# Kernel tuning notes

Measured on AMD Instinct MI355X. Metric: run time of the kernel, lower is better.

The kernel has to match this reference:

```python
import jax, jax.numpy as jnp
import numpy as np

WEIGHT = 1.0
TEMPERATURE = 1.0
POWER = 2.0
NEG_FILL = -1e9
EPS = 1e-8


def _cos_sim_matrix(x):
    # row-normalize then GEMM: equivalent to pairwise F.cosine_similarity
    norms = jnp.linalg.norm(x, axis=-1, keepdims=True)
    xn = x / jnp.maximum(norms, EPS)
    return xn @ xn.T  # [N, N]


def setup_inputs() -> dict:
    key = jax.random.key(0)
    k1, k2 = jax.random.split(key)
    model_output = jax.random.normal(k1, (8192, 512), dtype=jnp.float32)
    targets = jax.random.normal(k2, (8192, 768), dtype=jnp.float32)
    return {"model_output": model_output, "targets": targets}


def reference(model_output, targets):
    N = model_output.shape[0]
    eye = jnp.eye(N, dtype=bool)

    sim_o = jnp.where(eye, NEG_FILL, _cos_sim_matrix(model_output))
    sim_t = jnp.where(eye, NEG_FILL, _cos_sim_matrix(targets))

    student_log_probs = jax.nn.log_softmax(sim_o / TEMPERATURE, axis=-1)
    teacher_probs = jax.nn.softmax(sim_t / TEMPERATURE, axis=-1)

    weights = jax.lax.stop_gradient(teacher_probs ** POWER)

    # torch F.kl_div(input=log_p_student, target=p_teacher, reduction='none')
    # = where(target > 0, target * (log(target) - input), 0)
    tp_safe = jnp.where(teacher_probs > 0, teacher_probs, 1.0)
    kl = jnp.where(teacher_probs > 0,
                   teacher_probs * (jnp.log(tp_safe) - student_log_probs),
                   0.0)

    loss = jnp.mean(weights * kl)
    return WEIGHT * loss
```

## Files before the change

### kernel.cpp

```cpp
#include <hip/hip_runtime.h>

#define N    8192
#define DT   768
#define DO   512
#define BM   128
#define BN   128
#define TI   (N / BM)
#define TJ   (N / BN)
#define NTILE (TI * (TI + 1) / 2)
#define NSLOT (2 * TJ)
#define PL    ((size_t)NSLOT * N)
#define NKT   (DT / 32)
#define NKO   (DO / 32)

typedef __attribute__((ext_vector_type(8))) short   short8;
typedef __attribute__((ext_vector_type(4))) float   floatx4;

struct alignas(8) us4 { unsigned short x[4]; };

__device__ inline unsigned short f2bf(float x) {
    union { float f; unsigned int u; } v; v.f = x;
    unsigned int r = v.u + 0x7fffu + ((v.u >> 16) & 1u);
    return (unsigned short)(r >> 16);
}
__device__ inline float bf2f(unsigned short u) {
    union { unsigned int u; float f; } v; v.u = ((unsigned int)u) << 16;
    return v.f;
}

__device__ inline void gl2lds16(const unsigned short* g, unsigned short* l) {
    __builtin_amdgcn_global_load_lds(
        (const __attribute__((address_space(1))) unsigned int*)(const void*)g,
        (__attribute__((address_space(3))) unsigned int*)(void*)l,
        16, 0, 0);
}

template <int NKC>
__device__ inline void stage_packed(const unsigned short* __restrict__ P,
                                    unsigned short* sA, unsigned short* sB,
                                    int pi, int pj, int s, int t) {
    const unsigned short* bi = P + ((size_t)(pi * NKC + s) << 12);
    const unsigned short* bj = P + ((size_t)(pj * NKC + s) << 12);
    #pragma unroll
    for (int h = 0; h < 2; ++h) {
        const int idx = t + h * 256;
        gl2lds16(bi + idx * 8, &sA[idx * 8]);
        gl2lds16(bj + idx * 8, &sB[idx * 8]);
    }
}

__device__ inline void tile_coords(int bid, int& ti, int& tj) {
    int swb = (bid & 7) * (NTILE / 8) + (bid >> 3);
    int sti = 0, stj = 0;
    for (;;) {
        const int sz = (sti == stj) ? 36 : 64;
        if (swb < sz) break;
        swb -= sz;
        if (++stj == 8) { ++sti; stj = sti; }
    }
    int i, j;
    if (sti == stj) {
        i = 0;
        while (swb >= 8 - i) { swb -= 8 - i; ++i; }
        j = i + swb;
    } else {
        i = swb >> 3;
        j = swb & 7;
    }
    ti = sti * 8 + i;
    tj = stj * 8 + j;
}

__global__ void norm_kernel(const float* __restrict__ Tg,
                            const float* __restrict__ Mo,
                            unsigned short* __restrict__ Pt,
                            unsigned short* __restrict__ Po,
                            float* __restrict__ zero_me) {
    if (blockIdx.x == 0 && threadIdx.x == 0) zero_me[0] = 0.0f;
    int bid = blockIdx.x;
    const float* X; unsigned short* Pk; int D, NKC;
    if (bid < N / 4) { X = Tg; Pk = Pt; D = DT; NKC = NKT; }
    else             { bid -= N / 4; X = Mo; Pk = Po; D = DO; NKC = NKO; }
    const int row  = bid * 4 + (threadIdx.x >> 6);
    const int lane = threadIdx.x & 63;
    const int nch  = D >> 8;
    const int r    = row & 127;
    const int p    = row >> 7;
    const int key  = (r >> 1) & 3;
    const float* xr = X + (size_t)row * D;
    floatx4 vc[3];
    float ss = 0.0f;
    #pragma unroll
    for (int h = 0; h < 3; ++h) {
        if (h < nch) {
            vc[h] = *(const floatx4*)(xr + lane * 4 + h * 256);
            ss += vc[h][0] * vc[h][0] + vc[h][1] * vc[h][1]
                + vc[h][2] * vc[h][2] + vc[h][3] * vc[h][3];
        }
    }
    #pragma unroll
    for (int m = 32; m >= 1; m >>= 1) ss += __shfl_xor(ss, m);
    const float scale = 1.0f / fmaxf(sqrtf(ss), 1e-8f);
    #pragma unroll
    for (int h = 0; h < 3; ++h) {
        if (h < nch) {
            us4 o;
            #pragma unroll
            for (int j = 0; j < 4; ++j) o.x[j] = f2bf(vc[h][j] * scale);
            const int k0  = lane * 4 + h * 256;
            const int kc  = k0 >> 5;
            const int ch  = (k0 >> 3) & 3;
            const int cs  = ch ^ key;
            const int pos = (k0 >> 2) & 1;
            const size_t a = ((size_t)(p * NKC + kc) << 12)
                           + (size_t)(r * 4 + cs) * 8 + pos * 4;
            *(us4*)(Pk + a) = o;
        }
    }
}

__launch_bounds__(256, 3)
__global__ void fused_kernel(const unsigned short* __restrict__ Pt,
                             const unsigned short* __restrict__ Po,
                             float* __restrict__ partials) {
    __shared__ unsigned short sA[BM * 32];
    __shared__ unsigned short sB[BN * 32];
    __shared__ unsigned short sW[64 * 256];

    const int t    = threadIdx.x;
    const int lane = t & 63;
    const int w    = t >> 6;
    const int wm   = w >> 1, wn = w & 1;
    const int lr   = lane & 15, lg = lane >> 4;
    const int lgx  = lg ^ ((lr >> 1) & 3);

    int ti, tj; tile_coords(blockIdx.x, ti, tj);
    const bool offdiag = (ti != tj);
    const int i0 = ti * BM, j0 = tj * BN;

    floatx4 acc[4][4];
    #pragma unroll
    for (int a = 0; a < 4; ++a)
        #pragma unroll
        for (int b = 0; b < 4; ++b)
            acc[a][b] = (floatx4){0.0f, 0.0f, 0.0f, 0.0f};

    for (int s = 0; s < NKT; ++s) {
        stage_packed<NKT>(Pt, sA, sB, ti, tj, s, t);
        asm volatile("s_waitcnt vmcnt(0)" ::: "memory");
        __syncthreads();
        short8 af[4], bf[4];
        #pragma unroll
        for (int mi = 0; mi < 4; ++mi)
            af[mi] = *(const short8*)&sA[(wm * 64 + mi * 16 + lr) * 32 + (lgx << 3)];
        #pragma unroll
        for (int ni = 0; ni < 4; ++ni)
            bf[ni] = *(const short8*)&sB[(wn * 64 + ni * 16 + lr) * 32 + (lgx << 3)];
        #pragma unroll
        for (int mi = 0; mi < 4; ++mi)
            #pragma unroll
            for (int ni = 0; ni < 4; ++ni)
                acc[mi][ni] = __builtin_amdgcn_mfma_f32_16x16x32_bf16(
                    af[mi], bf[ni], acc[mi][ni], 0, 0, 0);
        __syncthreads();
    }

    {
        float czt[4], cvv[4], cua[4];
        #pragma unroll
        for (int ni = 0; ni < 4; ++ni) { czt[ni] = 0.0f; cvv[ni] = 0.0f; cua[ni] = 0.0f; }
        #pragma unroll
        for (int mi = 0; mi < 4; ++mi) {
            #pragma unroll
            for (int r = 0; r < 4; ++r) {
                const int row = wm * 64 + mi * 16 + lg * 4 + r;
                const int gi  = i0 + row;
                float zt = 0.0f, vv = 0.0f, ua = 0.0f;
                #pragma unroll
                for (int ni = 0; ni < 4; ++ni) {
                    const int gj = j0 + wn * 64 + ni * 16 + lr;
                    const float a = acc[mi][ni][r];
                    float ea = __expf(a - 1.0f);
                    if (gi == gj) ea = 0.0f;
                    const float e3 = ea * ea * ea;
                    zt += ea; vv += e3; ua += e3 * a;
                    czt[ni] += ea; cvv[ni] += e3; cua[ni] += e3 * a;
                    sW[(mi * 16 + ni * 4 + r) * 256 + t] = f2bf(e3);
                }
                #pragma unroll
                for (int m = 8; m >= 1; m >>= 1) {
                    zt += __shfl_xor(zt, m);
                    vv += __shfl_xor(vv, m);
                    ua += __shfl_xor(ua, m);
                }
                if (lr == 0) {
                    const size_t base = (size_t)(tj * 2 + wn) * N + gi;
                    partials[0 * PL + base] = zt;
                    partials[1 * PL + base] = vv;
                    partials[2 * PL + base] = ua;
                }
            }
        }
        if (offdiag) {
            #pragma unroll
            for (int ni = 0; ni < 4; ++ni) {
                #pragma unroll
                for (int m = 16; m <= 32; m <<= 1) {
                    czt[ni] += __shfl_xor(czt[ni], m);
                    cvv[ni] += __shfl_xor(cvv[ni], m);
                    cua[ni] += __shfl_xor(cua[ni], m);
                }
            }
            if (lg == 0) {
                #pragma unroll
                for (int ni = 0; ni < 4; ++ni) {
                    const int gj = j0 + wn * 64 + ni * 16 + lr;
                    const size_t base = (size_t)(ti * 2 + wm) * N + gj;
                    partials[0 * PL + base] = czt[ni];
                    partials[1 * PL + base] = cvv[ni];
                    partials[2 * PL + base] = cua[ni];
                }
            }
        }
    }

    #pragma unroll
    for (int a = 0; a < 4; ++a)
        #pragma unroll
        for (int b = 0; b < 4; ++b)
            acc[a][b] = (floatx4){0.0f, 0.0f, 0.0f, 0.0f};

    for (int s = 0; s < NKO; ++s) {
        stage_packed<NKO>(Po, sA, sB, ti, tj, s, t);
        asm volatile("s_waitcnt vmcnt(0)" ::: "memory");
        __syncthreads();
        short8 af[4], bf[4];
        #pragma unroll
        for (int mi = 0; mi < 4; ++mi)
            af[mi] = *(const short8*)&sA[(wm * 64 + mi * 16 + lr) * 32 + (lgx << 3)];
        #pragma unroll
        for (int ni = 0; ni < 4; ++ni)
            bf[ni] = *(const short8*)&sB[(wn * 64 + ni * 16 + lr) * 32 + (lgx << 3)];
        #pragma unroll
        for (int mi = 0; mi < 4; ++mi)
            #pragma unroll
            for (int ni = 0; ni < 4; ++ni)
                acc[mi][ni] = __builtin_amdgcn_mfma_f32_16x16x32_bf16(
                    af[mi], bf[ni], acc[mi][ni], 0, 0, 0);
        __syncthreads();
    }

    {
        float czo[4], cwb[4];
        #pragma unroll
        for (int ni = 0; ni < 4; ++ni) { czo[ni] = 0.0f; cwb[ni] = 0.0f; }
        #pragma unroll
        for (int mi = 0; mi < 4; ++mi) {
            #pragma unroll
            for (int r = 0; r < 4; ++r) {
                const int row = wm * 64 + mi * 16 + lg * 4 + r;
                const int gi  = i0 + row;
                float zo = 0.0f, wb = 0.0f;
                #pragma unroll
                for (int ni = 0; ni < 4; ++ni) {
                    const int gj = j0 + wn * 64 + ni * 16 + lr;
                    const float b = acc[mi][ni][r];
                    float eb = __expf(b - 1.0f);
                    if (gi == gj) eb = 0.0f;
                    const float wgt = bf2f(sW[(mi * 16 + ni * 4 + r) * 256 + t]);
                    zo += eb; wb += wgt * b;
                    czo[ni] += eb; cwb[ni] += wgt * b;
                }
                #pragma unroll
                for (int m = 8; m >= 1; m >>= 1) {
                    zo += __shfl_xor(zo, m);
                    wb += __shfl_xor(wb, m);
                }
                if (lr == 0) {
                    const size_t base = (size_t)(tj * 2 + wn) * N + gi;
                    partials[3 * PL + base] = zo;
                    partials[4 * PL + base] = wb;
                }
            }
        }
        if (offdiag) {
            #pragma unroll
            for (int ni = 0; ni < 4; ++ni) {
                #pragma unroll
                for (int m = 16; m <= 32; m <<= 1) {
                    czo[ni] += __shfl_xor(czo[ni], m);
                    cwb[ni] += __shfl_xor(cwb[ni], m);
                }
            }
            if (lg == 0) {
                #pragma unroll
                for (int ni = 0; ni < 4; ++ni) {
                    const int gj = j0 + wn * 64 + ni * 16 + lr;
                    const size_t base = (size_t)(ti * 2 + wm) * N + gj;
                    partials[3 * PL + base] = czo[ni];
                    partials[4 * PL + base] = cwb[ni];
                }
            }
        }
    }
}

__global__ void reduce_kernel(const float* __restrict__ partials,
                              float* __restrict__ out) {
    __shared__ float sh[5][256];
    const int t    = threadIdx.x;
    const int lane = t & 63;
    const int g    = t >> 6;
    const int i    = blockIdx.x * 64 + lane;
    float s[5] = {0.0f, 0.0f, 0.0f, 0.0f, 0.0f};
    for (int jb = g * (NSLOT / 4); jb < (g + 1) * (NSLOT / 4); ++jb) {
        const size_t base = (size_t)jb * N + i;
        #pragma unroll
        for (int p = 0; p < 5; ++p) s[p] += partials[p * PL + base];
    }
    #pragma unroll
    for (int p = 0; p < 5; ++p) sh[p][t] = s[p];
    __syncthreads();
    if (g == 0) {
        float v[5];
        #pragma unroll
        for (int p = 0; p < 5; ++p)
            v[p] = sh[p][lane] + sh[p][64 + lane] + sh[p][128 + lane] + sh[p][192 + lane];
        float li = (v[2] - v[4] + v[1] * __logf(v[3] / v[0])) / (v[0] * v[0] * v[0]);
        #pragma unroll
        for (int m = 32; m >= 1; m >>= 1) li += __shfl_xor(li, m);
        if (lane == 0)
            atomicAdd(out, li * (1.0f / ((float)N * (float)N)));
    }
}

extern "C" void kernel_launch(void* const* d_in, const int* in_sizes, int n_in,
                              void* d_out, int out_size, void* d_ws, size_t ws_size,
                              hipStream_t stream) {
    (void)in_sizes; (void)n_in; (void)out_size; (void)ws_size;
    const float* mo = (const float*)d_in[0];
    const float* tg = (const float*)d_in[1];
    float* out = (float*)d_out;

    char* ws = (char*)d_ws;
    unsigned short* Pt = (unsigned short*)ws;
    unsigned short* Po = (unsigned short*)(ws + (size_t)N * DT * 2);
    float* partials    = (float*)(ws + (size_t)N * DT * 2 + (size_t)N * DO * 2);

    norm_kernel<<<2 * (N / 4), 256, 0, stream>>>(tg, mo, Pt, Po, out);
    fused_kernel<<<NTILE, 256, 0, stream>>>(Pt, Po, partials);
    reduce_kernel<<<N / 64, 256, 0, stream>>>(partials, out);
}
```

Before: 283.9 us.

## Double-buffer LDS stages across both GEMMs and keep half of weights in registers

Turns the single-buffered K loop into a double-buffered pipeline that starts the next global-to-LDS load before the current MFMA step. It also chains the targets GEMM straight into the model-output GEMM, so the first output stage is prefetched during the last targets step. The extra A/B buffer is paid for by halving the LDS weight scratch and holding the other half of the bf16 weights packed in 16 registers. This raises register pressure, which under launch_bounds(256,3) could cause spills, and it relies on a single barrier per step for correctness.

Result: slower. 321.0 us (+13.1%).

```diff
diff --git a/kernel.cpp b/kernel.cpp
--- a/kernel.cpp
+++ b/kernel.cpp
@@ -12,6 +12,7 @@
 #define PL    ((size_t)NSLOT * N)
 #define NKT   (DT / 32)
 #define NKO   (DO / 32)
+#define NSTEP (NKT + NKO)
 
 typedef __attribute__((ext_vector_type(8))) short   short8;
 typedef __attribute__((ext_vector_type(4))) float   floatx4;
@@ -123,9 +124,9 @@
 __global__ void fused_kernel(const unsigned short* __restrict__ Pt,
                              const unsigned short* __restrict__ Po,
                              float* __restrict__ partials) {
-    __shared__ unsigned short sA[BM * 32];
-    __shared__ unsigned short sB[BN * 32];
-    __shared__ unsigned short sW[64 * 256];
+    __shared__ unsigned short sA[2][BM * 32];
+    __shared__ unsigned short sB[2][BN * 32];
+    __shared__ unsigned short sWl[32 * 256];
 
     const int t    = threadIdx.x;
     const int lane = t & 63;
@@ -138,6 +139,7 @@
     const bool offdiag = (ti != tj);
     const int i0 = ti * BM, j0 = tj * BN;
 
+    unsigned int w3p[16];
     floatx4 acc[4][4];
     #pragma unroll
     for (int a = 0; a < 4; ++a)
@@ -145,24 +147,37 @@
         for (int b = 0; b < 4; ++b)
             acc[a][b] = (floatx4){0.0f, 0.0f, 0.0f, 0.0f};
 
-    for (int s = 0; s < NKT; ++s) {
-        stage_packed<NKT>(Pt, sA, sB, ti, tj, s, t);
-        asm volatile("s_waitcnt vmcnt(0)" ::: "memory");
-        __syncthreads();
+    auto stage_any = [&](int u) {
+        unsigned short* a = sA[u & 1];
+        unsigned short* b = sB[u & 1];
+        if (u < NKT) stage_packed<NKT>(Pt, a, b, ti, tj, u, t);
+        else         stage_packed<NKO>(Po, a, b, ti, tj, u - NKT, t);
+    };
+
+    auto mfma_step = [&](const unsigned short* sAb, const unsigned short* sBb) {
         short8 af[4], bf[4];
         #pragma unroll
         for (int mi = 0; mi < 4; ++mi)
-            af[mi] = *(const short8*)&sA[(wm * 64 + mi * 16 + lr) * 32 + (lgx << 3)];
+            af[mi] = *(const short8*)&sAb[(wm * 64 + mi * 16 + lr) * 32 + (lgx << 3)];
         #pragma unroll
         for (int ni = 0; ni < 4; ++ni)
-            bf[ni] = *(const short8*)&sB[(wn * 64 + ni * 16 + lr) * 32 + (lgx << 3)];
+            bf[ni] = *(const short8*)&sBb[(wn * 64 + ni * 16 + lr) * 32 + (lgx << 3)];
         #pragma unroll
         for (int mi = 0; mi < 4; ++mi)
             #pragma unroll
             for (int ni = 0; ni < 4; ++ni)
                 acc[mi][ni] = __builtin_amdgcn_mfma_f32_16x16x32_bf16(
                     af[mi], bf[ni], acc[mi][ni], 0, 0, 0);
-        __syncthreads();
+    };
+
+    stage_any(0);
+    for (int s = 0; s < NKT; ++s) {
+        asm volatile("s_waitcnt vmcnt(0)" ::: "memory");
+        __builtin_amdgcn_s_barrier();
+        asm volatile("" ::: "memory");
+        stage_any(s + 1);
+        mfma_step(sA[s & 1], sB[s & 1]);
+        asm volatile("" ::: "memory");
     }
 
     {
@@ -185,7 +200,14 @@
                     const float e3 = ea * ea * ea;
                     zt += ea; vv += e3; ua += e3 * a;
                     czt[ni] += ea; cvv[ni] += e3; cua[ni] += e3 * a;
-                    sW[(mi * 16 + ni * 4 + r) * 256 + t] = f2bf(e3);
+                    const int idx = mi * 16 + ni * 4 + r;
+                    if (idx < 32) {
+                        sWl[idx * 256 + t] = f2bf(e3);
+                    } else {
+                        const int q = (idx - 32) >> 1;
+                        if (idx & 1) w3p[q] |= ((unsigned int)f2bf(e3)) << 16;
+                        else         w3p[q]  = (unsigned int)f2bf(e3);
+                    }
                 }
                 #pragma unroll
                 for (int m = 8; m >= 1; m >>= 1) {
@@ -230,24 +252,13 @@
         for (int b = 0; b < 4; ++b)
             acc[a][b] = (floatx4){0.0f, 0.0f, 0.0f, 0.0f};
 
-    for (int s = 0; s < NKO; ++s) {
-        stage_packed<NKO>(Po, sA, sB, ti, tj, s, t);
+    for (int s = NKT; s < NSTEP; ++s) {
         asm volatile("s_waitcnt vmcnt(0)" ::: "memory");
-        __syncthreads();
-        short8 af[4], bf[4];
-        #pragma unroll
-        for (int mi = 0; mi < 4; ++mi)
-            af[mi] = *(const short8*)&sA[(wm * 64 + mi * 16 + lr) * 32 + (lgx << 3)];
-        #pragma unroll
-        for (int ni = 0; ni < 4; ++ni)
-            bf[ni] = *(const short8*)&sB[(wn * 64 + ni * 16 + lr) * 32 + (lgx << 3)];
-        #pragma unroll
-        for (int mi = 0; mi < 4; ++mi)
-            #pragma unroll
-            for (int ni = 0; ni < 4; ++ni)
-                acc[mi][ni] = __builtin_amdgcn_mfma_f32_16x16x32_bf16(
-                    af[mi], bf[ni], acc[mi][ni], 0, 0, 0);
-        __syncthreads();
+        __builtin_amdgcn_s_barrier();
+        asm volatile("" ::: "memory");
+        if (s + 1 < NSTEP) stage_any(s + 1);
+        mfma_step(sA[s & 1], sB[s & 1]);
+        asm volatile("" ::: "memory");
     }
 
     {
@@ -267,7 +278,15 @@
                     const float b = acc[mi][ni][r];
                     float eb = __expf(b - 1.0f);
                     if (gi == gj) eb = 0.0f;
-                    const float wgt = bf2f(sW[(mi * 16 + ni * 4 + r) * 256 + t]);
+                    const int idx = mi * 16 + ni * 4 + r;
+                    float wgt;
+                    if (idx < 32) {
+                        wgt = bf2f(sWl[idx * 256 + t]);
+                    } else {
+                        const unsigned int pw = w3p[(idx - 32) >> 1];
+                        wgt = bf2f((unsigned short)((idx & 1) ? (pw >> 16)
+                                                              : (pw & 0xffffu)));
+                    }
                     zo += eb; wb += wgt * b;
                     czo[ni] += eb; cwb[ni] += wgt * b;
                 }
```
